# Kernel tuning notes

Hardware: AMD Instinct MI355X
Metric: run time of the kernel (lower is better)

The kernel has to match this reference:

```python
import jax, jax.numpy as jnp
import numpy as np

NHEAD = 4
DIM = 256

def rotate_half(x):
    # interleaved: out[..., ::2] = -x[..., 1::2]; out[..., 1::2] = x[..., ::2]
    xe = x[..., ::2]
    xo = x[..., 1::2]
    return jnp.stack([-xo, xe], axis=-1).reshape(x.shape)

def rope_2d(q, k, H, W):
    Dh = q.shape[-1]
    half = Dh // 2
    inv_freq = 1.0 / (10000.0 ** (jnp.arange(half, dtype=jnp.float32) / half))  # [half]
    yy, xx = jnp.meshgrid(jnp.arange(H, dtype=jnp.float32), jnp.arange(W, dtype=jnp.float32), indexing='ij')
    ang_y = yy.reshape(-1)[:, None] * inv_freq  # [N, half]
    ang_x = xx.reshape(-1)[:, None] * inv_freq  # [N, half]
    cy, sy = jnp.cos(ang_y), jnp.sin(ang_y)
    cx, sx = jnp.cos(ang_x), jnp.sin(ang_x)
    def rot(t):
        t1 = t[..., :half]          # y-rotated half
        t2 = t[..., half:2 * half]  # x-rotated half
        ty = t1 * cy + rotate_half(t1) * sy
        tx = t2 * cx + rotate_half(t2) * sx
        return jnp.concatenate([ty, tx, t[..., 2 * half:]], axis=-1)
    return rot(q), rot(k)

def layernorm(x, g, b, eps=1e-5):
    mu = jnp.mean(x, axis=-1, keepdims=True)
    var = jnp.var(x, axis=-1, keepdims=True)
    return (x - mu) / jnp.sqrt(var + eps) * g + b

def setup_inputs() -> dict:
    key = jax.random.key(0)
    ks = jax.random.split(key, 8)
    B, Hs, Ws, C = 4, 48, 48, DIM
    N = Hs * Ws
    s = 0.02
    return {
        'x': jax.random.normal(ks[0], (B, N, C), dtype=jnp.float32),
        'Wqkv': jax.random.normal(ks[1], (3 * C, C), dtype=jnp.float32) * s,
        'Wproj': jax.random.normal(ks[2], (C, C), dtype=jnp.float32) * s,
        'g1': jnp.ones((C,), jnp.float32), 'b1': jnp.zeros((C,), jnp.float32),
        'g2': jnp.ones((C,), jnp.float32), 'b2': jnp.zeros((C,), jnp.float32),
        'W1': jax.random.normal(ks[3], (4 * C, C), dtype=jnp.float32) * s,
        'bf1': jnp.zeros((4 * C,), jnp.float32),
        'W2': jax.random.normal(ks[4], (C, 4 * C), dtype=jnp.float32) * s,
        'bf2': jnp.zeros((C,), jnp.float32),
        'H': Hs, 'W': Ws,
    }

def reference(x, Wqkv, Wproj, g1, b1, g2, b2, W1, bf1, W2, bf2, H, W):
    B, N, C = x.shape
    dh = C // NHEAD
    qkv = (x @ Wqkv.T).reshape(B, N, 3, NHEAD, dh).transpose(2, 0, 3, 1, 4)  # [3,B,h,N,dh]
    q, k, v = qkv[0], qkv[1], qkv[2]
    q, k = rope_2d(q, k, H, W)
    scores = jnp.einsum('bhnd,bhmd->bhnm', q, k) / jnp.sqrt(jnp.float32(dh))
    attn = jax.nn.softmax(scores, axis=-1)  # drop_attn is identity (p=0)
    out = jnp.einsum('bhnm,bhmd->bhnd', attn, v).transpose(0, 2, 1, 3).reshape(B, N, C)
    x = x + out @ Wproj.T
    x = layernorm(x, g1, b1)
    h = jax.nn.gelu(x @ W1.T + bf1, approximate=False)
    x = x + h @ W2.T + bf2
    return layernorm(x, g2, b2)
```

## Files before the change

### kernel.cpp

```cpp
#include <hip/hip_runtime.h>
#include <hip/hip_bf16.h>
#include <math.h>

typedef __hip_bfloat16 bf16;
typedef __attribute__((ext_vector_type(8))) short short8;
typedef __attribute__((ext_vector_type(4))) short short4v;
typedef __attribute__((ext_vector_type(4))) float f32x4;
typedef __attribute__((ext_vector_type(4))) unsigned int u32x4;

#define NSEQ 2304
#define CDIM 256
#define NHD  4
#define DH   64

#if __has_builtin(__builtin_amdgcn_exp2f)
#define EXP2F __builtin_amdgcn_exp2f
#else
#define EXP2F exp2f
#endif

static __device__ __forceinline__ f32x4 mfma_bf16(short8 a, short8 b, f32x4 c) {
  return __builtin_amdgcn_mfma_f32_16x16x32_bf16(a, b, c, 0, 0, 0);
}
static __device__ __forceinline__ short8 ld8(const bf16* p) {
  return *reinterpret_cast<const short8*>(p);
}
static __device__ __forceinline__ short8 lds8(const bf16* p) {
  return *reinterpret_cast<const short8*>(p);
}
static __device__ __forceinline__ float b2f(short v) {
  unsigned int u = ((unsigned int)(unsigned short)v) << 16;
  return __uint_as_float(u);
}
static __device__ __forceinline__ short f2b(float f) {
  bf16 h = __float2bfloat16(f);
  return *reinterpret_cast<short*>(&h);
}

__global__ __launch_bounds__(256) void detect_kernel(const void* __restrict__ xraw,
                                                     int* __restrict__ flag) {
  int t = threadIdx.x;
  const unsigned short* s = (const unsigned short*)xraw;
  int bad = 0;
#pragma unroll
  for (int i = 0; i < 8; ++i) {
    unsigned idx = (((unsigned)(t * 8 + i)) * 9173u) & ((1u << 20) - 1);
    unsigned short v = s[idx * 2];
    unsigned e = (v >> 7) & 0xFFu;
    if (e > 133u) bad++;
  }
  __shared__ int tot;
  if (t == 0) tot = 0;
  __syncthreads();
  atomicAdd(&tot, bad);
  __syncthreads();
  if (t == 0) flag[0] = (tot >= 16) ? 1 : 0;
}

__global__ __launch_bounds__(256) void cvt_all_kernel(const void* sx, const void* sqkv, const void* sproj,
                                                      const void* sw1, const void* sw2,
                                                      const void* g1, const void* b1, const void* g2,
                                                      const void* b2, const void* bias1, const void* bias2,
                                                      bf16* dx, bf16* dqkv, bf16* dproj,
                                                      bf16* dw1, bf16* dw2, bf16* dsm,
                                                      const int* __restrict__ flag) {
  int is32 = flag[0];
  int bid = blockIdx.x;
  const void* src; bf16* dst; int i4;
  if (bid < 2304)      { src = sx;    dst = dx;    i4 = bid * 256 + threadIdx.x; }
  else if (bid < 2496) { src = sqkv;  dst = dqkv;  i4 = (bid - 2304) * 256 + threadIdx.x; }
  else if (bid < 2560) { src = sproj; dst = dproj; i4 = (bid - 2496) * 256 + threadIdx.x; }
  else if (bid < 2816) { src = sw1;   dst = dw1;   i4 = (bid - 2560) * 256 + threadIdx.x; }
  else if (bid < 3072) { src = sw2;   dst = dw2;   i4 = (bid - 2816) * 256 + threadIdx.x; }
  else {
    const void* srcs[6] = {g1, b1, g2, b2, bias1, bias2};
    const int ns[6] = {256, 256, 256, 256, 1024, 256};
    const int off[6] = {0, 256, 512, 768, 1024, 2048};
    int t = threadIdx.x;
#pragma unroll
    for (int j = 0; j < 6; ++j)
      for (int i = t; i < ns[j]; i += 256) {
        if (is32) dsm[off[j] + i] = __float2bfloat16(((const float*)srcs[j])[i]);
        else      dsm[off[j] + i] = ((const bf16*)srcs[j])[i];
      }
    return;
  }
  if (is32) {
    float4 v = ((const float4*)src)[i4];
    short4v o;
    o[0] = f2b(v.x); o[1] = f2b(v.y); o[2] = f2b(v.z); o[3] = f2b(v.w);
    ((short4v*)dst)[i4] = o;
  } else {
    ((short4v*)dst)[i4] = ((const short4v*)src)[i4];
  }
}

__global__ __launch_bounds__(256, 1) void qkv_kernel(const bf16* __restrict__ X,
                                                     const bf16* __restrict__ Wqkv,
                                                     bf16* __restrict__ Q, bf16* __restrict__ K,
                                                     bf16* __restrict__ Vt,
                                                     const int* __restrict__ Wp) {
  int wave = threadIdx.x >> 6, lane = threadIdx.x & 63;
  int l15 = lane & 15, quad = lane >> 4;
  int m0 = (blockIdx.x * 4 + wave) * 64;
  int n0 = blockIdx.y * 64;
  const bf16* arow = X + (size_t)(m0 + l15) * CDIM + quad * 8;
  const bf16* brow = Wqkv + (size_t)(n0 + l15) * CDIM + quad * 8;
  f32x4 z = {0.f, 0.f, 0.f, 0.f};
  f32x4 acc[4][4];
#pragma unroll
  for (int j = 0; j < 4; ++j)
#pragma unroll
    for (int i = 0; i < 4; ++i) acc[j][i] = z;

  short8 a[4], b[4];
#pragma unroll
  for (int i = 0; i < 4; ++i) a[i] = ld8(arow + (size_t)i * 16 * CDIM);
#pragma unroll
  for (int j = 0; j < 4; ++j) b[j] = ld8(brow + (size_t)j * 16 * CDIM);
#pragma unroll
  for (int kk = 32; kk <= CDIM; kk += 32) {
    short8 an[4], bn[4];
    if (kk < CDIM) {
#pragma unroll
      for (int i = 0; i < 4; ++i) an[i] = ld8(arow + (size_t)i * 16 * CDIM + kk);
#pragma unroll
      for (int j = 0; j < 4; ++j) bn[j] = ld8(brow + (size_t)j * 16 * CDIM + kk);
    }
#pragma unroll
    for (int j = 0; j < 4; ++j)
#pragma unroll
      for (int i = 0; i < 4; ++i) acc[j][i] = mfma_bf16(b[j], a[i], acc[j][i]);
    if (kk < CDIM) {
#pragma unroll
      for (int i = 0; i < 4; ++i) a[i] = an[i];
#pragma unroll
      for (int j = 0; j < 4; ++j) b[j] = bn[j];
    }
  }

  int which = n0 >> 8, h = (n0 & 255) >> 6;
  if (which == 2) {
#pragma unroll
    for (int j = 0; j < 4; ++j) {
      int d0 = j * 16 + quad * 4;
#pragma unroll
      for (int i = 0; i < 4; ++i) {
        int gm = m0 + i * 16 + l15;
        int bb = gm / NSEQ, n = gm % NSEQ;
        int bh = bb * NHD + h;
#pragma unroll
        for (int r = 0; r < 4; ++r)
          Vt[((size_t)bh * DH + d0 + r) * NSEQ + n] = __float2bfloat16(acc[j][i][r]);
      }
    }
  } else {
    int Wv = Wp[0];
    if (Wv <= 0 || Wv > 65536) Wv = 48;
    bf16* dst = (which == 0) ? Q : K;
    const float cc = -0.28782313662425574f;
    const float EC1 = 0.7498942434f, EC2 = 0.5623413252f, EC3 = 0.4216965034f;
#pragma unroll
    for (int i = 0; i < 4; ++i) {
      int gm = m0 + i * 16 + l15;
      int bb = gm / NSEQ, n = gm % NSEQ;
      int bh = bb * NHD + h;
      int py = n / Wv, px = n - py * Wv;
#pragma unroll
      for (int j = 0; j < 4; ++j) {
        int d0 = j * 16 + quad * 4;
        float pos = (d0 & 32) ? (float)px : (float)py;
        int base = d0 & 31;
        float fb = __expf(cc * (float)base);
        float f0 = fb, f1 = fb * EC1, f2 = fb * EC2, f3 = fb * EC3;
        float s0, c0, s1, c1, s2, c2, s3, c3;
        __sincosf(pos * f0, &s0, &c0);
        __sincosf(pos * f1, &s1, &c1);
        __sincosf(pos * f2, &s2, &c2);
        __sincosf(pos * f3, &s3, &c3);
        float a0 = acc[j][i][0], a1 = acc[j][i][1], a2 = acc[j][i][2], a3 = acc[j][i][3];
        short4v ov;
        ov[0] = f2b(a0 * c0 - a1 * s0);
        ov[1] = f2b(a1 * c1 + a0 * s1);
        ov[2] = f2b(a2 * c2 - a3 * s2);
        ov[3] = f2b(a3 * c3 + a2 * s3);
        *reinterpret_cast<short4v*>(dst + ((size_t)bh * NSEQ + n) * DH + d0) = ov;
      }
    }
  }
}

__global__ __launch_bounds__(256, 4) void attn_kernel(const bf16* __restrict__ Q, const bf16* __restrict__ K,
                                                      const bf16* __restrict__ Vt, bf16* __restrict__ AO) {
  int bh = blockIdx.x, qt = blockIdx.y;
  int tid = threadIdx.x;
  int wave = tid >> 6, lane = tid & 63;
  int l15 = lane & 15, quad = lane >> 4;
  int qf = wave & 1;
  int ks = wave >> 1;
  int m0 = qt * 64 + qf * 32;
  const bf16* Qb = Q + (size_t)bh * NSEQ * DH;
  const bf16* Kb = K + (size_t)bh * NSEQ * DH;
  const bf16* Vb = Vt + (size_t)bh * DH * NSEQ;

  __shared__ __align__(16) bf16 kbuf[2][64 * 72];
  __shared__ __align__(16) bf16 vbuf[2][64 * 72];

  int r1 = tid >> 3, c1 = (tid & 7) * 8;
  int r1b = r1 + 32;

  const float QS = 0.18033688011112042f;
  short8 qa0 = ld8(Qb + (size_t)(m0 + l15) * DH + quad * 8);
  short8 qa1 = ld8(Qb + (size_t)(m0 + l15) * DH + 32 + quad * 8);
  short8 qb0 = ld8(Qb + (size_t)(m0 + 16 + l15) * DH + quad * 8);
  short8 qb1 = ld8(Qb + (size_t)(m0 + 16 + l15) * DH + 32 + quad * 8);
#pragma unroll
  for (int i = 0; i < 8; ++i) {
    qa0[i] = f2b(b2f(qa0[i]) * QS);
    qa1[i] = f2b(b2f(qa1[i]) * QS);
    qb0[i] = f2b(b2f(qb0[i]) * QS);
    qb1[i] = f2b(b2f(qb1[i]) * QS);
  }

  f32x4 z = {0.f, 0.f, 0.f, 0.f};
  f32x4 o[4] = {z, z, z, z};
  f32x4 o2[4] = {z, z, z, z};
  float l_run = 0.f, l_run2 = 0.f;

  *reinterpret_cast<short8*>(kbuf[0] + r1 * 72 + c1)  = ld8(Kb + (size_t)r1 * DH + c1);
  *reinterpret_cast<short8*>(kbuf[0] + r1b * 72 + c1) = ld8(Kb + (size_t)r1b * DH + c1);
  *reinterpret_cast<short8*>(vbuf[0] + r1 * 72 + c1)  = ld8(Vb + (size_t)r1 * NSEQ + c1);
  *reinterpret_cast<short8*>(vbuf[0] + r1b * 72 + c1) = ld8(Vb + (size_t)r1b * NSEQ + c1);
  __syncthreads();

  for (int it = 0; it < NSEQ / 64; ++it) {
    int cur = it & 1;
    bool more = (it + 1 < NSEQ / 64);

    short8 kpA, kpB, vpA, vpB;
    if (more) {
      int kn = (it + 1) * 64;
      kpA = ld8(Kb + (size_t)(kn + r1) * DH + c1);
      kpB = ld8(Kb + (size_t)(kn + r1b) * DH + c1);
      vpA = ld8(Vb + (size_t)r1 * NSEQ + kn + c1);
      vpB = ld8(Vb + (size_t)r1b * NSEQ + kn + c1);
    }

    const bf16* kb = kbuf[cur];
    const bf16* vb = vbuf[cur];

    f32x4 s[2], s2[2];
#pragma unroll
    for (int kt = 0; kt < 2; ++kt) {
      const bf16* kp = kb + (size_t)(ks * 32 + kt * 16 + l15) * 72 + quad * 8;
      short8 kf0 = lds8(kp);
      short8 kf1 = lds8(kp + 32);
      s[kt] = mfma_bf16(kf0, qa0, z);
      s[kt] = mfma_bf16(kf1, qa1, s[kt]);
      s2[kt] = mfma_bf16(kf0, qb0, z);
      s2[kt] = mfma_bf16(kf1, qb1, s2[kt]);
    }

    unsigned int A0, B0, A1, B1, C0, D0, C1, D1;
    {
      float p00 = EXP2F(s[0][0]), p01 = EXP2F(s[0][1]), p02 = EXP2F(s[0][2]), p03 = EXP2F(s[0][3]);
      float p10 = EXP2F(s[1][0]), p11 = EXP2F(s[1][1]), p12 = EXP2F(s[1][2]), p13 = EXP2F(s[1][3]);
      l_run += ((p00 + p01) + (p02 + p03)) + ((p10 + p11) + (p12 + p13));
      asm("v_cvt_pk_bf16_f32 %0, %1, %2" : "=v"(A0) : "v"(p00), "v"(p01));
      asm("v_cvt_pk_bf16_f32 %0, %1, %2" : "=v"(B0) : "v"(p02), "v"(p03));
      asm("v_cvt_pk_bf16_f32 %0, %1, %2" : "=v"(A1) : "v"(p10), "v"(p11));
      asm("v_cvt_pk_bf16_f32 %0, %1, %2" : "=v"(B1) : "v"(p12), "v"(p13));
      float q00 = EXP2F(s2[0][0]), q01 = EXP2F(s2[0][1]), q02 = EXP2F(s2[0][2]), q03 = EXP2F(s2[0][3]);
      float q10 = EXP2F(s2[1][0]), q11 = EXP2F(s2[1][1]), q12 = EXP2F(s2[1][2]), q13 = EXP2F(s2[1][3]);
      l_run2 += ((q00 + q01) + (q02 + q03)) + ((q10 + q11) + (q12 + q13));
      asm("v_cvt_pk_bf16_f32 %0, %1, %2" : "=v"(C0) : "v"(q00), "v"(q01));
      asm("v_cvt_pk_bf16_f32 %0, %1, %2" : "=v"(D0) : "v"(q02), "v"(q03));
      asm("v_cvt_pk_bf16_f32 %0, %1, %2" : "=v"(C1) : "v"(q10), "v"(q11));
      asm("v_cvt_pk_bf16_f32 %0, %1, %2" : "=v"(D1) : "v"(q12), "v"(q13));
    }
    asm("v_permlane32_swap_b32 %0, %1" : "+v"(A0), "+v"(A1));
    asm("v_permlane16_swap_b32 %0, %1" : "+v"(A0), "+v"(A1));
    asm("v_permlane32_swap_b32 %0, %1" : "+v"(B0), "+v"(B1));
    asm("v_permlane16_swap_b32 %0, %1" : "+v"(B0), "+v"(B1));
    asm("v_permlane32_swap_b32 %0, %1" : "+v"(C0), "+v"(C1));
    asm("v_permlane16_swap_b32 %0, %1" : "+v"(C0), "+v"(C1));
    asm("v_permlane32_swap_b32 %0, %1" : "+v"(D0), "+v"(D1));
    asm("v_permlane16_swap_b32 %0, %1" : "+v"(D0), "+v"(D1));

    u32x4 wA; wA[0] = A0; wA[1] = B0; wA[2] = A1; wA[3] = B1;
    u32x4 wB; wB[0] = C0; wB[1] = D0; wB[2] = C1; wB[3] = D1;
    short8 pfA = *reinterpret_cast<short8*>(&wA);
    short8 pfB = *reinterpret_cast<short8*>(&wB);

#pragma unroll
    for (int t = 0; t < 4; ++t) {
      short8 vf = lds8(vb + (size_t)(t * 16 + l15) * 72 + ks * 32 + quad * 8);
      o[t] = mfma_bf16(vf, pfA, o[t]);
      o2[t] = mfma_bf16(vf, pfB, o2[t]);
    }

    if (more) {
      bf16* kn_ = kbuf[1 - cur];
      bf16* vn_ = vbuf[1 - cur];
      *reinterpret_cast<short8*>(kn_ + r1 * 72 + c1)  = kpA;
      *reinterpret_cast<short8*>(kn_ + r1b * 72 + c1) = kpB;
      *reinterpret_cast<short8*>(vn_ + r1 * 72 + c1)  = vpA;
      *reinterpret_cast<short8*>(vn_ + r1b * 72 + c1) = vpB;
    }
    __syncthreads();
  }

  float* scr = (float*)kbuf;
  int slot = qf * 64 + lane;
  if (ks == 1) {
    float* p = scr + slot * 36;
#pragma unroll
    for (int t = 0; t < 4; ++t) {
      *reinterpret_cast<f32x4*>(p + t * 4) = o[t];
      *reinterpret_cast<f32x4*>(p + 16 + t * 4) = o2[t];
    }
    p[32] = l_run;
    p[33] = l_run2;
  }
  __syncthreads();
  if (ks == 0) {
    float* p = scr + slot * 36;
#pragma unroll
    for (int t = 0; t < 4; ++t) {
      f32x4 pa = *reinterpret_cast<f32x4*>(p + t * 4);
      f32x4 pb2 = *reinterpret_cast<f32x4*>(p + 16 + t * 4);
#pragma unroll
      for (int r = 0; r < 4; ++r) {
        o[t][r] += pa[r];
        o2[t][r] += pb2[r];
      }
    }
    l_run += p[32];
    l_run2 += p[33];

    l_run += __shfl_xor(l_run, 16);
    l_run += __shfl_xor(l_run, 32);
    l_run2 += __shfl_xor(l_run2, 16);
    l_run2 += __shfl_xor(l_run2, 32);
    float inv = 1.f / l_run;
    float inv2 = 1.f / l_run2;
    int b = bh >> 2, h = bh & 3;
    bf16* orow = AO + ((size_t)b * NSEQ + (m0 + l15)) * CDIM + h * DH;
    bf16* orow2 = AO + ((size_t)b * NSEQ + (m0 + 16 + l15)) * CDIM + h * DH;
#pragma unroll
    for (int t = 0; t < 4; ++t) {
      short4v ov, ov2;
#pragma unroll
      for (int r = 0; r < 4; ++r) {
        ov[r] = f2b(o[t][r] * inv);
        ov2[r] = f2b(o2[t][r] * inv2);
      }
      *reinterpret_cast<short4v*>(orow + t * 16 + quad * 4) = ov;
      *reinterpret_cast<short4v*>(orow2 + t * 16 + quad * 4) = ov2;
    }
  }
}

template <int KD, int EPI, int TI>
__global__ __launch_bounds__(256) void gemm128(const bf16* __restrict__ A, const bf16* __restrict__ Wm,
                                               const bf16* __restrict__ bias, const bf16* __restrict__ res,
                                               bf16* __restrict__ outp, int NC) {
  constexpr int KS = KD / 32;
  constexpr int AR = TI * 32;
  int tid = threadIdx.x;
  int wave = tid >> 6, lane = tid & 63;
  int l15 = lane & 15, quad = lane >> 4;
  int wm = (wave >> 1) * (TI * 16);
  int wn = (wave & 1) * 64;
  int m0 = blockIdx.x * AR;
  int n0 = blockIdx.y * 128;

  __shared__ __align__(16) bf16 abuf[2][AR * 40];
  __shared__ __align__(16) bf16 bbuf[2][128 * 40];

  int sr = tid >> 2, sc = (tid & 3) * 8;

  const bf16* ag[TI / 2];
#pragma unroll
  for (int u = 0; u < TI / 2; ++u) ag[u] = A + (size_t)(m0 + sr + u * 64) * KD + sc;
  const bf16* bg0 = Wm + (size_t)(n0 + sr) * KD + sc;
  const bf16* bg1 = Wm + (size_t)(n0 + 64 + sr) * KD + sc;

  f32x4 z = {0.f, 0.f, 0.f, 0.f};
  f32x4 acc[4][TI];
#pragma unroll
  for (int j = 0; j < 4; ++j)
#pragma unroll
    for (int i = 0; i < TI; ++i) acc[j][i] = z;

#pragma unroll
  for (int u = 0; u < TI / 2; ++u)
    *reinterpret_cast<short8*>(abuf[0] + (sr + u * 64) * 40 + sc) = ld8(ag[u]);
  *reinterpret_cast<short8*>(bbuf[0] + sr * 40 + sc) = ld8(bg0);
  *reinterpret_cast<short8*>(bbuf[0] + (64 + sr) * 40 + sc) = ld8(bg1);
  __syncthreads();

  for (int s = 0; s < KS; ++s) {
    int cur = s & 1;
    bool more = (s + 1 < KS);
    short8 anx[TI / 2], bnx0, bnx1;
    if (more) {
#pragma unroll
      for (int u = 0; u < TI / 2; ++u) anx[u] = ld8(ag[u] + (s + 1) * 32);
      bnx0 = ld8(bg0 + (s + 1) * 32);
      bnx1 = ld8(bg1 + (s + 1) * 32);
    }
    short8 af[TI], bf_[4];
#pragma unroll
    for (int i = 0; i < TI; ++i)
      af[i] = lds8(abuf[cur] + (size_t)(wm + i * 16 + l15) * 40 + quad * 8);
#pragma unroll
    for (int j = 0; j < 4; ++j)
      bf_[j] = lds8(bbuf[cur] + (size_t)(wn + j * 16 + l15) * 40 + quad * 8);
#pragma unroll
    for (int j = 0; j < 4; ++j)
#pragma unroll
      for (int i = 0; i < TI; ++i)
        acc[j][i] = mfma_bf16(bf_[j], af[i], acc[j][i]);
    if (more) {
#pragma unroll
      for (int u = 0; u < TI / 2; ++u)
        *reinterpret_cast<short8*>(abuf[1 - cur] + (sr + u * 64) * 40 + sc) = anx[u];
      *reinterpret_cast<short8*>(bbuf[1 - cur] + sr * 40 + sc) = bnx0;
      *reinterpret_cast<short8*>(bbuf[1 - cur] + (64 + sr) * 40 + sc) = bnx1;
    }
    __syncthreads();
  }

#pragma unroll
  for (int j = 0; j < 4; ++j) {
    int col0 = n0 + wn + j * 16 + quad * 4;
    float bb4[4];
    if (EPI != 0) {
      short4v bl = *reinterpret_cast<const short4v*>(bias + col0);
#pragma unroll
      for (int r = 0; r < 4; ++r) bb4[r] = b2f(bl[r]);
    }
#pragma unroll
    for (int i = 0; i < TI; ++i) {
      size_t idx = (size_t)(m0 + wm + i * 16 + l15) * NC + col0;
      short4v ov;
      if (EPI == 0) {
        short4v rl = *reinterpret_cast<const short4v*>(res + idx);
#pragma unroll
        for (int r = 0; r < 4; ++r) ov[r] = f2b(acc[j][i][r] + b2f(rl[r]));
      } else if (EPI == 1) {
#pragma unroll
        for (int r = 0; r < 4; ++r) {
          float hv = acc[j][i][r] + bb4[r];
          ov[r] = f2b(0.5f * hv * (1.f + erff(hv * 0.70710678118f)));
        }
      } else {
        short4v rl = *reinterpret_cast<const short4v*>(res + idx);
#pragma unroll
        for (int r = 0; r < 4; ++r) ov[r] = f2b(acc[j][i][r] + bb4[r] + b2f(rl[r]));
      }
      *reinterpret_cast<short4v*>(outp + idx) = ov;
    }
  }
}

__global__ __launch_bounds__(256) void ln_kernel(const bf16* __restrict__ X, const bf16* __restrict__ g,
                                                 const bf16* __restrict__ bv, bf16* __restrict__ out) {
  int row = blockIdx.x * 4 + (threadIdx.x >> 6);
  int lane = threadIdx.x & 63;
  short4v raw = *reinterpret_cast<const short4v*>(X + (size_t)row * CDIM + lane * 4);
  float vv[4];
  float s = 0.f, sq = 0.f;
#pragma unroll
  for (int i = 0; i < 4; ++i) {
    float f = b2f(raw[i]);
    vv[i] = f; s += f; sq += f * f;
  }
#pragma unroll
  for (int off = 1; off < 64; off <<= 1) { s += __shfl_xor(s, off); sq += __shfl_xor(sq, off); }
  float mu = s * (1.f / CDIM);
  float var = sq * (1.f / CDIM) - mu * mu;
  float rstd = rsqrtf(var + 1e-5f);
#pragma unroll
  for (int i = 0; i < 4; ++i) {
    int c = lane * 4 + i;
    out[(size_t)row * CDIM + c] =
        __float2bfloat16((vv[i] - mu) * rstd * __bfloat162float(g[c]) + __bfloat162float(bv[c]));
  }
}

__global__ __launch_bounds__(256) void ln_out_kernel(const bf16* __restrict__ X, const bf16* __restrict__ g,
                                                     const bf16* __restrict__ bv, void* __restrict__ out,
                                                     const int* __restrict__ flag) {
  int is32 = flag[0];
  int row = blockIdx.x * 4 + (threadIdx.x >> 6);
  int lane = threadIdx.x & 63;
  short4v raw = *reinterpret_cast<const short4v*>(X + (size_t)row * CDIM + lane * 4);
  float vv[4];
  float s = 0.f, sq = 0.f;
#pragma unroll
  for (int i = 0; i < 4; ++i) {
    float f = b2f(raw[i]);
    vv[i] = f; s += f; sq += f * f;
  }
#pragma unroll
  for (int off = 1; off < 64; off <<= 1) { s += __shfl_xor(s, off); sq += __shfl_xor(sq, off); }
  float mu = s * (1.f / CDIM);
  float var = sq * (1.f / CDIM) - mu * mu;
  float rstd = rsqrtf(var + 1e-5f);
#pragma unroll
  for (int i = 0; i < 4; ++i) {
    int c = lane * 4 + i;
    size_t idx = (size_t)row * CDIM + c;
    float v = (vv[i] - mu) * rstd * __bfloat162float(g[c]) + __bfloat162float(bv[c]);
    if (is32) ((float*)out)[idx] = v;
    else      ((bf16*)out)[idx] = __float2bfloat16(v);
  }
}

extern "C" void kernel_launch(void* const* d_in, const int* in_sizes, int n_in,
                              void* d_out, int out_size, void* d_ws, size_t ws_size,
                              hipStream_t stream) {
  const int* Wp = (const int*)d_in[12];

  char* ws = (char*)d_ws;
  const size_t SZ = 4718592;
  bf16* Qc  = (bf16*)(ws + 0 * SZ);
  bf16* Kc  = (bf16*)(ws + 1 * SZ);
  bf16* Vt  = (bf16*)(ws + 2 * SZ);
  bf16* AO  = (bf16*)(ws + 3 * SZ);
  bf16* F   = (bf16*)(ws + 4 * SZ);
  bf16* Y   = (bf16*)(ws + 5 * SZ);
  bf16* xc  = (bf16*)(ws + 6 * SZ);
  bf16* G   = (bf16*)(ws + 0);
  bf16* Wqkvc  = (bf16*)(ws + 7 * SZ);
  bf16* Wprojc = (bf16*)(ws + 7 * SZ + 393216);
  bf16* W1c    = (bf16*)(ws + 7 * SZ + 524288);
  bf16* W2c    = (bf16*)(ws + 7 * SZ + 1048576);
  bf16* smallc = (bf16*)(ws + 7 * SZ + 1572864);
  bf16* g1c  = smallc + 0;
  bf16* b1c  = smallc + 256;
  bf16* g2c  = smallc + 512;
  bf16* b2c  = smallc + 768;
  bf16* bf1c = smallc + 1024;
  bf16* bf2c = smallc + 2048;
  int*  flagp = (int*)(ws + 7 * SZ + 1581568);
  bf16* outsc = (bf16*)d_out;

  detect_kernel<<<1, 256, 0, stream>>>(d_in[0], flagp);
  cvt_all_kernel<<<3073, 256, 0, stream>>>(d_in[0], d_in[1], d_in[2], d_in[7], d_in[9],
                                           d_in[3], d_in[4], d_in[5], d_in[6], d_in[8], d_in[10],
                                           xc, Wqkvc, Wprojc, W1c, W2c, smallc, flagp);

  qkv_kernel<<<dim3(36, 12), 256, 0, stream>>>(xc, Wqkvc, Qc, Kc, Vt, Wp);
  attn_kernel<<<dim3(16, 36), 256, 0, stream>>>(Qc, Kc, Vt, AO);
  gemm128<256, 0, 2><<<dim3(144, 2), 256, 0, stream>>>(AO, Wprojc, nullptr, xc, outsc, 256);
  ln_kernel<<<2304, 256, 0, stream>>>(outsc, g1c, b1c, F);
  gemm128<256, 1, 4><<<dim3(72, 8), 256, 0, stream>>>(F, W1c, bf1c, nullptr, G, 1024);
  gemm128<1024, 2, 2><<<dim3(144, 2), 256, 0, stream>>>(G, W2c, bf2c, F, Y, 256);
  ln_out_kernel<<<2304, 256, 0, stream>>>(Y, g2c, b2c, d_out, flagp);
}
```

Baseline: 207.7 us.

## Fuse residual-add LayerNorm into the projection and FFN-down GEMM epilogues

Replaces the two N=256 GEMMs and their separate LayerNorm kernels with a new gemm_ln kernel. Each block computes a full 32x256 row tile, so the row mean and variance can be reduced in registers and shared memory, and the normalized output is written directly. This removes two kernel launches and the round trip of the intermediate activation through global memory. The cost is smaller M tiles (32 rows, 288 blocks), less weight reuse per block, and an extra sync for the cross-wave reduction.

New measurement: 205.3 us. Within noise of the previous version (-1.1%).

```diff
diff --git a/kernel.cpp b/kernel.cpp
--- a/kernel.cpp
+++ b/kernel.cpp
@@ -465,57 +465,143 @@
   }
 }
 
-__global__ __launch_bounds__(256) void ln_kernel(const bf16* __restrict__ X, const bf16* __restrict__ g,
-                                                 const bf16* __restrict__ bv, bf16* __restrict__ out) {
-  int row = blockIdx.x * 4 + (threadIdx.x >> 6);
-  int lane = threadIdx.x & 63;
-  short4v raw = *reinterpret_cast<const short4v*>(X + (size_t)row * CDIM + lane * 4);
-  float vv[4];
-  float s = 0.f, sq = 0.f;
-#pragma unroll
-  for (int i = 0; i < 4; ++i) {
-    float f = b2f(raw[i]);
-    vv[i] = f; s += f; sq += f * f;
-  }
-#pragma unroll
-  for (int off = 1; off < 64; off <<= 1) { s += __shfl_xor(s, off); sq += __shfl_xor(sq, off); }
-  float mu = s * (1.f / CDIM);
-  float var = sq * (1.f / CDIM) - mu * mu;
-  float rstd = rsqrtf(var + 1e-5f);
-#pragma unroll
-  for (int i = 0; i < 4; ++i) {
-    int c = lane * 4 + i;
-    out[(size_t)row * CDIM + c] =
-        __float2bfloat16((vv[i] - mu) * rstd * __bfloat162float(g[c]) + __bfloat162float(bv[c]));
-  }
-}
-
-__global__ __launch_bounds__(256) void ln_out_kernel(const bf16* __restrict__ X, const bf16* __restrict__ g,
-                                                     const bf16* __restrict__ bv, void* __restrict__ out,
-                                                     const int* __restrict__ flag) {
-  int is32 = flag[0];
-  int row = blockIdx.x * 4 + (threadIdx.x >> 6);
-  int lane = threadIdx.x & 63;
-  short4v raw = *reinterpret_cast<const short4v*>(X + (size_t)row * CDIM + lane * 4);
-  float vv[4];
-  float s = 0.f, sq = 0.f;
-#pragma unroll
-  for (int i = 0; i < 4; ++i) {
-    float f = b2f(raw[i]);
-    vv[i] = f; s += f; sq += f * f;
-  }
-#pragma unroll
-  for (int off = 1; off < 64; off <<= 1) { s += __shfl_xor(s, off); sq += __shfl_xor(sq, off); }
-  float mu = s * (1.f / CDIM);
-  float var = sq * (1.f / CDIM) - mu * mu;
-  float rstd = rsqrtf(var + 1e-5f);
-#pragma unroll
-  for (int i = 0; i < 4; ++i) {
-    int c = lane * 4 + i;
-    size_t idx = (size_t)row * CDIM + c;
-    float v = (vv[i] - mu) * rstd * __bfloat162float(g[c]) + __bfloat162float(bv[c]);
-    if (is32) ((float*)out)[idx] = v;
-    else      ((bf16*)out)[idx] = __float2bfloat16(v);
+template <int KD, int HASBIAS, int FINAL>
+__global__ __launch_bounds__(256) void gemm_ln(const bf16* __restrict__ A, const bf16* __restrict__ Wm,
+                                               const bf16* __restrict__ bias, const bf16* __restrict__ res,
+                                               const bf16* __restrict__ g, const bf16* __restrict__ bv,
+                                               void* __restrict__ outp, const int* __restrict__ flag) {
+  constexpr int KS = KD / 32;
+  int tid = threadIdx.x;
+  int wave = tid >> 6, lane = tid & 63;
+  int l15 = lane & 15, quad = lane >> 4;
+  int wn = wave * 64;
+  int m0 = blockIdx.x * 32;
+  int is32 = FINAL ? flag[0] : 0;
+
+  __shared__ __align__(16) bf16 abuf[2][32 * 40];
+  __shared__ __align__(16) bf16 bbuf[2][256 * 40];
+  __shared__ float red[4][32][2];
+
+  int sr = tid >> 2, sc = (tid & 3) * 8;
+  bool doA = tid < 128;
+  int ra = tid >> 2, ca = (tid & 3) * 8;
+
+  const bf16* ag = A + (size_t)(m0 + ra) * KD + ca;
+  const bf16* bg[4];
+#pragma unroll
+  for (int u = 0; u < 4; ++u) bg[u] = Wm + (size_t)(sr + u * 64) * KD + sc;
+
+  f32x4 z = {0.f, 0.f, 0.f, 0.f};
+  f32x4 acc[4][2];
+#pragma unroll
+  for (int j = 0; j < 4; ++j)
+#pragma unroll
+    for (int i = 0; i < 2; ++i) acc[j][i] = z;
+
+  if (doA) *reinterpret_cast<short8*>(abuf[0] + ra * 40 + ca) = ld8(ag);
+#pragma unroll
+  for (int u = 0; u < 4; ++u)
+    *reinterpret_cast<short8*>(bbuf[0] + (sr + u * 64) * 40 + sc) = ld8(bg[u]);
+  __syncthreads();
+
+  for (int s = 0; s < KS; ++s) {
+    int cur = s & 1;
+    bool more = (s + 1 < KS);
+    short8 anx, bnx[4];
+    if (more) {
+      if (doA) anx = ld8(ag + (s + 1) * 32);
+#pragma unroll
+      for (int u = 0; u < 4; ++u) bnx[u] = ld8(bg[u] + (s + 1) * 32);
+    }
+    short8 af[2], bf_[4];
+#pragma unroll
+    for (int i = 0; i < 2; ++i)
+      af[i] = lds8(abuf[cur] + (size_t)(i * 16 + l15) * 40 + quad * 8);
+#pragma unroll
+    for (int j = 0; j < 4; ++j)
+      bf_[j] = lds8(bbuf[cur] + (size_t)(wn + j * 16 + l15) * 40 + quad * 8);
+#pragma unroll
+    for (int j = 0; j < 4; ++j)
+#pragma unroll
+      for (int i = 0; i < 2; ++i)
+        acc[j][i] = mfma_bf16(bf_[j], af[i], acc[j][i]);
+    if (more) {
+      if (doA) *reinterpret_cast<short8*>(abuf[1 - cur] + ra * 40 + ca) = anx;
+#pragma unroll
+      for (int u = 0; u < 4; ++u)
+        *reinterpret_cast<short8*>(bbuf[1 - cur] + (sr + u * 64) * 40 + sc) = bnx[u];
+    }
+    __syncthreads();
+  }
+
+  float bb[4][4];
+  if (HASBIAS) {
+#pragma unroll
+    for (int j = 0; j < 4; ++j) {
+      short4v bl = *reinterpret_cast<const short4v*>(bias + wn + j * 16 + quad * 4);
+#pragma unroll
+      for (int r = 0; r < 4; ++r) bb[j][r] = b2f(bl[r]);
+    }
+  }
+  float vals[2][4][4];
+  float s0 = 0.f, q0 = 0.f, s1 = 0.f, q1 = 0.f;
+#pragma unroll
+  for (int i = 0; i < 2; ++i) {
+    int row = m0 + i * 16 + l15;
+#pragma unroll
+    for (int j = 0; j < 4; ++j) {
+      int col0 = wn + j * 16 + quad * 4;
+      short4v rl = *reinterpret_cast<const short4v*>(res + (size_t)row * CDIM + col0);
+#pragma unroll
+      for (int r = 0; r < 4; ++r) {
+        float v = acc[j][i][r] + (HASBIAS ? bb[j][r] : 0.f) + b2f(rl[r]);
+        vals[i][j][r] = v;
+        if (i == 0) { s0 += v; q0 += v * v; }
+        else        { s1 += v; q1 += v * v; }
+      }
+    }
+  }
+  s0 += __shfl_xor(s0, 16); s0 += __shfl_xor(s0, 32);
+  q0 += __shfl_xor(q0, 16); q0 += __shfl_xor(q0, 32);
+  s1 += __shfl_xor(s1, 16); s1 += __shfl_xor(s1, 32);
+  q1 += __shfl_xor(q1, 16); q1 += __shfl_xor(q1, 32);
+  if (quad == 0) {
+    red[wave][l15][0] = s0;      red[wave][l15][1] = q0;
+    red[wave][16 + l15][0] = s1; red[wave][16 + l15][1] = q1;
+  }
+  __syncthreads();
+
+#pragma unroll
+  for (int i = 0; i < 2; ++i) {
+    int rl_ = i * 16 + l15;
+    float S = 0.f, Q = 0.f;
+#pragma unroll
+    for (int w = 0; w < 4; ++w) { S += red[w][rl_][0]; Q += red[w][rl_][1]; }
+    float mu = S * (1.f / CDIM);
+    float var = Q * (1.f / CDIM) - mu * mu;
+    float rstd = rsqrtf(var + 1e-5f);
+    int row = m0 + i * 16 + l15;
+#pragma unroll
+    for (int j = 0; j < 4; ++j) {
+      int col0 = wn + j * 16 + quad * 4;
+      short4v gl = *reinterpret_cast<const short4v*>(g + col0);
+      short4v bl2 = *reinterpret_cast<const short4v*>(bv + col0);
+      size_t idx = (size_t)row * CDIM + col0;
+      if (FINAL && is32) {
+        float4 ov;
+        ov.x = (vals[i][j][0] - mu) * rstd * b2f(gl[0]) + b2f(bl2[0]);
+        ov.y = (vals[i][j][1] - mu) * rstd * b2f(gl[1]) + b2f(bl2[1]);
+        ov.z = (vals[i][j][2] - mu) * rstd * b2f(gl[2]) + b2f(bl2[2]);
+        ov.w = (vals[i][j][3] - mu) * rstd * b2f(gl[3]) + b2f(bl2[3]);
+        *reinterpret_cast<float4*>((float*)outp + idx) = ov;
+      } else {
+        short4v ov;
+#pragma unroll
+        for (int r = 0; r < 4; ++r)
+          ov[r] = f2b((vals[i][j][r] - mu) * rstd * b2f(gl[r]) + b2f(bl2[r]));
+        *reinterpret_cast<short4v*>((bf16*)outp + idx) = ov;
+      }
+    }
   }
 }
 
@@ -531,7 +617,6 @@
   bf16* Vt  = (bf16*)(ws + 2 * SZ);
   bf16* AO  = (bf16*)(ws + 3 * SZ);
   bf16* F   = (bf16*)(ws + 4 * SZ);
-  bf16* Y   = (bf16*)(ws + 5 * SZ);
   bf16* xc  = (bf16*)(ws + 6 * SZ);
   bf16* G   = (bf16*)(ws + 0);
   bf16* Wqkvc  = (bf16*)(ws + 7 * SZ);
@@ -546,7 +631,6 @@
   bf16* bf1c = smallc + 1024;
   bf16* bf2c = smallc + 2048;
   int*  flagp = (int*)(ws + 7 * SZ + 1581568);
-  bf16* outsc = (bf16*)d_out;
 
   detect_kernel<<<1, 256, 0, stream>>>(d_in[0], flagp);
   cvt_all_kernel<<<3073, 256, 0, stream>>>(d_in[0], d_in[1], d_in[2], d_in[7], d_in[9],
@@ -555,9 +639,7 @@
 
   qkv_kernel<<<dim3(36, 12), 256, 0, stream>>>(xc, Wqkvc, Qc, Kc, Vt, Wp);
   attn_kernel<<<dim3(16, 36), 256, 0, stream>>>(Qc, Kc, Vt, AO);
-  gemm128<256, 0, 2><<<dim3(144, 2), 256, 0, stream>>>(AO, Wprojc, nullptr, xc, outsc, 256);
-  ln_kernel<<<2304, 256, 0, stream>>>(outsc, g1c, b1c, F);
+  gemm_ln<256, 0, 0><<<288, 256, 0, stream>>>(AO, Wprojc, nullptr, xc, g1c, b1c, F, flagp);
   gemm128<256, 1, 4><<<dim3(72, 8), 256, 0, stream>>>(F, W1c, bf1c, nullptr, G, 1024);
-  gemm128<1024, 2, 2><<<dim3(144, 2), 256, 0, stream>>>(G, W2c, bf2c, F, Y, 256);
-  ln_out_kernel<<<2304, 256, 0, stream>>>(Y, g2c, b2c, d_out, flagp);
-}
+  gemm_ln<1024, 1, 1><<<288, 256, 0, stream>>>(G, W2c, bf2c, F, g2c, b2c, d_out, flagp);
+}
```
